# Performance work log

Hardware: AMD Instinct MI355X
Metric: run time of the kernel (lower is better)

The kernel has to match this reference:

```python
import jax, jax.numpy as jnp
import numpy as np
import math

NUM_HEADS = 16


def _alibi_slopes(num_heads: int):
    # geometric sequence for power-of-2 head counts (paper's scheme)
    def slopes_pow2(n):
        start = 2.0 ** (-(2.0 ** (-(math.log2(n) - 3))))
        return [start * (start ** i) for i in range(n)]
    if math.log2(num_heads).is_integer():
        return slopes_pow2(num_heads)
    c = 2 ** math.floor(math.log2(num_heads))
    extra = slopes_pow2(2 * c)[0::2][: num_heads - c]
    return slopes_pow2(c) + extra


def setup_inputs() -> dict:
    key = jax.random.key(0)
    kq, kk, kv = jax.random.split(key, 3)
    B, H, S, D = 2, NUM_HEADS, 2048, 64
    q = jax.random.normal(kq, (B, H, S, D), dtype=jnp.float32)
    k = jax.random.normal(kk, (B, H, S, D), dtype=jnp.float32)
    v = jax.random.normal(kv, (B, H, S, D), dtype=jnp.float32)
    return {"q": q, "k": k, "v": v}


def reference(q, k, v):
    B, H, Sq, D = q.shape
    Sk = k.shape[2]
    slopes = jnp.asarray(_alibi_slopes(H), dtype=jnp.float32)  # [H]
    pos = jnp.arange(Sk)
    # abs relative positions (symmetric, non-causal) as in the source
    rel = jnp.abs(pos[None, :] - pos[:, None]).astype(jnp.float32)  # [Sk, Sk]
    alibi = -slopes[:, None, None] * rel[None, :Sq, :]  # [H, Sq, Sk]
    scores = jnp.einsum("bhqd,bhkd->bhqk", q, k) / math.sqrt(D)
    scores = scores + alibi[None]
    probs = jax.nn.softmax(scores, axis=-1)
    return jnp.einsum("bhqk,bhkd->bhqd", probs, v)
```

## Files before the change

kernel.cpp:

```cpp
#include <hip/hip_runtime.h>
#include <hip/hip_bf16.h>
#include <math.h>

typedef __bf16 bf16;
typedef __attribute__((ext_vector_type(8))) bf16 bf16x8;
typedef __attribute__((ext_vector_type(2))) bf16 bf16x2;
typedef __attribute__((ext_vector_type(16))) float f32x16;
typedef __attribute__((ext_vector_type(4))) unsigned int uint4v;

#define SQ 2048
#define DH 64
#define NH 16
#define KVT 32
#define NKVT (SQ / KVT)
#define REC 8192
#define LOG2E 1.44269504088896340736f
#define NITEMS 1024
#define GRID 640
#define THETA 14.0f

__device__ __forceinline__ float fast_exp2(float x) {
#if __has_builtin(__builtin_amdgcn_exp2f)
    return __builtin_amdgcn_exp2f(x);
#else
    return exp2f(x);
#endif
}

__device__ __forceinline__ unsigned pkbf16(float a, float b) {
    union { bf16x2 h; unsigned u; } x;
    x.h = (bf16x2){(bf16)a, (bf16)b};
    return x.u;
}

#if __has_builtin(__builtin_amdgcn_permlane32_swap)
__device__ __forceinline__ void plswap(unsigned &a, unsigned &b) {
    typedef __attribute__((ext_vector_type(2))) unsigned int uint2v;
    uint2v r = __builtin_amdgcn_permlane32_swap(a, b, false, false);
    a = r[0]; b = r[1];
}
#else
__device__ __forceinline__ void plswap(unsigned &a, unsigned &b) {
    asm volatile("v_permlane32_swap_b32 %0, %1" : "+v"(a), "+v"(b));
}
#endif

union FragU { uint4v u; bf16x8 b; };

__global__ __launch_bounds__(256)
void alibi_prep_kernel(const float* __restrict__ K, const float* __restrict__ V,
                       char* __restrict__ W, int* __restrict__ ctr) {
    __shared__ bf16 lt[64][80];
    const int t  = threadIdx.x;
    const int s0 = blockIdx.x * 64;
    const int bh = blockIdx.y;
    if (ctr && blockIdx.x == 0 && blockIdx.y == 0 && blockIdx.z == 0 && t == 0)
        *ctr = 0;
    if (blockIdx.z == 0) {
#pragma unroll
        for (int i = 0; i < 2; ++i) {
            const int g    = i * 256 + t;
            const int tile = g >> 8;
            const int cc   = g & 255;
            const int ds   = cc >> 6;
            const int lane = cc & 63;
            const float* p = K + ((size_t)bh * SQ + s0 + tile * 32 + (lane & 31)) * DH
                               + ds * 16 + (lane >> 5) * 8;
            float4 a = *(const float4*)p, b = *(const float4*)(p + 4);
            bf16x8 pk = {(bf16)a.x,(bf16)a.y,(bf16)a.z,(bf16)a.w,
                         (bf16)b.x,(bf16)b.y,(bf16)b.z,(bf16)b.w};
            *(bf16x8*)(W + (size_t)(bh * NKVT + (s0 >> 5) + tile) * REC
                         + ds * 1024 + lane * 16) = pk;
        }
    } else {
#pragma unroll
        for (int i = 0; i < 2; ++i) {
            int idx = i * 256 + t;
            int row = idx >> 3, c8 = idx & 7;
            const float* p = V + ((size_t)bh * SQ + s0 + row) * DH + c8 * 8;
            float4 a = *(const float4*)p, b = *(const float4*)(p + 4);
            bf16 e[8] = {(bf16)a.x,(bf16)a.y,(bf16)a.z,(bf16)a.w,
                         (bf16)b.x,(bf16)b.y,(bf16)b.z,(bf16)b.w};
#pragma unroll
            for (int jj = 0; jj < 8; ++jj) lt[c8 * 8 + jj][row] = e[jj];
        }
        __syncthreads();
#pragma unroll
        for (int i = 0; i < 2; ++i) {
            const int g    = i * 256 + t;
            const int tile = g >> 8;
            const int cc   = g & 255;
            const int grp  = cc >> 6;
            const int lane = cc & 63;
            const int d    = (grp >> 1) * 32 + (lane & 31);
            const int sv   = tile * 32 + (grp & 1) * 16 + (lane >> 5) * 8;
            bf16x8 v = *(const bf16x8*)&lt[d][sv];
            *(bf16x8*)(W + (size_t)(bh * NKVT + (s0 >> 5) + tile) * REC
                         + 4096 + grp * 1024 + lane * 16) = v;
        }
    }
}

__global__ __launch_bounds__(256, 2)
void alibi_attn_kernel(const float* __restrict__ Q, const char* __restrict__ W,
                       float* __restrict__ Out, int* __restrict__ ctr) {
    __shared__ float ex[2][64][72];
    __shared__ int s_id;
    const int tid  = threadIdx.x;
    const int lane = tid & 63;
    const int par  = tid >> 6;
    const int r32  = lane & 31;
    const int hi   = lane >> 5;
    const float QSCALE = 0.125f * LOG2E;

    int next_static = blockIdx.x;

    while (true) {
        if (tid == 0) s_id = ctr ? atomicAdd(ctr, 1) : next_static;
        __syncthreads();
        const int r = s_id;
        next_static += GRID;
        if (r >= NITEMS) break;

        const int h   = 15 - (r >> 6);
        const int sub = r & 63;
        const int bh  = (sub >> 5) * NH + h;
        const int q0  = (sub & 31) * 64;

        const float slope2  = exp2f(-0.5f * (float)(h + 1)) * LOG2E;
        const float SLOPE2N = -slope2;
        const int D = (int)(THETA / slope2);
        const int a0 = q0 - D;
        const int tmin = (a0 <= 0) ? 0 : (a0 >> 5);
        const int tmax = min(NKVT - 1, (q0 + 63 + D) >> 5);

        const float* Qp = Q + (size_t)bh * SQ * DH;
        float*       Op = Out + (size_t)bh * SQ * DH;
        const char*  rec = W + (size_t)bh * NKVT * REC;

        const int qrowA = q0 + r32;
        bf16x8 qfragA[4], qfragB[4];
#pragma unroll
        for (int ds = 0; ds < 4; ++ds) {
            const float* sa = Qp + (size_t)qrowA * DH + ds * 16 + hi * 8;
            float4 a = *(const float4*)sa, b = *(const float4*)(sa + 4);
            qfragA[ds] = (bf16x8){(bf16)(a.x*QSCALE),(bf16)(a.y*QSCALE),
                                  (bf16)(a.z*QSCALE),(bf16)(a.w*QSCALE),
                                  (bf16)(b.x*QSCALE),(bf16)(b.y*QSCALE),
                                  (bf16)(b.z*QSCALE),(bf16)(b.w*QSCALE)};
            const float* sb = sa + 32 * DH;
            float4 c = *(const float4*)sb, d = *(const float4*)(sb + 4);
            qfragB[ds] = (bf16x8){(bf16)(c.x*QSCALE),(bf16)(c.y*QSCALE),
                                  (bf16)(c.z*QSCALE),(bf16)(c.w*QSCALE),
                                  (bf16)(d.x*QSCALE),(bf16)(d.y*QSCALE),
                                  (bf16)(d.z*QSCALE),(bf16)(d.w*QSCALE)};
        }

        f32x16 oaccA[2], oaccB[2];
#pragma unroll
        for (int d2 = 0; d2 < 2; ++d2)
#pragma unroll
            for (int rr = 0; rr < 16; ++rr) { oaccA[d2][rr] = 0.f; oaccB[d2][rr] = 0.f; }
        float psA[4] = {0.f,0.f,0.f,0.f}, psB[4] = {0.f,0.f,0.f,0.f};
        const float qhA = (float)(qrowA - 4 * hi);

        auto LOADF = [&](bf16x8* kf, bf16x8* vf, int tt) {
            const char* rb = rec + (size_t)tt * REC + lane * 16;
#pragma unroll
            for (int ds = 0; ds < 4; ++ds) kf[ds] = *(const bf16x8*)(rb + ds * 1024);
#pragma unroll
            for (int g = 0; g < 4; ++g)    vf[g] = *(const bf16x8*)(rb + 4096 + g * 1024);
        };

        auto COMPUTE = [&](const bf16x8* kf, const bf16x8* vf, int tt) {
            const float gq0 = qhA - (float)(tt * KVT);
#pragma unroll
            for (int qs = 0; qs < 2; ++qs) {
                const bf16x8* qf = qs ? qfragB : qfragA;
                f32x16*       oa = qs ? oaccB  : oaccA;
                float*        ps = qs ? psB    : psA;
                const float   gq = qs ? gq0 + 32.f : gq0;

                f32x16 sacc;
#pragma unroll
                for (int rr = 0; rr < 16; ++rr) sacc[rr] = 0.f;
                __builtin_amdgcn_s_setprio(1);
#pragma unroll
                for (int ds = 0; ds < 4; ++ds)
                    sacc = __builtin_amdgcn_mfma_f32_32x32x16_bf16(kf[ds], qf[ds], sacc, 0, 0, 0);
                __builtin_amdgcn_s_setprio(0);

                float p[16];
#pragma unroll
                for (int reg = 0; reg < 16; ++reg) {
                    const int krel = (reg & 3) + 8 * (reg >> 2);
                    float d = gq - (float)krel;
                    float s2 = fmaf(SLOPE2N, fabsf(d), sacc[reg]);
                    float e = fast_exp2(s2);
                    p[reg] = e;
                    ps[reg & 3] += e;
                }

                __builtin_amdgcn_s_setprio(1);
#pragma unroll
                for (int ks = 0; ks < 2; ++ks) {
                    unsigned u0 = pkbf16(p[8 * ks + 0], p[8 * ks + 1]);
                    unsigned u1 = pkbf16(p[8 * ks + 2], p[8 * ks + 3]);
                    unsigned v0 = pkbf16(p[8 * ks + 4], p[8 * ks + 5]);
                    unsigned v1 = pkbf16(p[8 * ks + 6], p[8 * ks + 7]);
                    plswap(u0, v0);
                    plswap(u1, v1);
                    FragU pf; pf.u = (uint4v){u0, u1, v0, v1};
#pragma unroll
                    for (int dblk = 0; dblk < 2; ++dblk)
                        oa[dblk] = __builtin_amdgcn_mfma_f32_32x32x16_bf16(vf[dblk * 2 + ks], pf.b, oa[dblk], 0, 0, 0);
                }
                __builtin_amdgcn_s_setprio(0);
            }
        };

        {
            bf16x8 kA[4], vA[4], kB[4], vB[4];
            int t = tmin + par;
            if (t <= tmax) {
                const int n = ((tmax - t) >> 2) + 1;
                LOADF(kA, vA, t);
                int i = 0;
                while (i + 2 <= n) {
                    LOADF(kB, vB, t + 4);
                    asm volatile("s_waitcnt vmcnt(8)" ::: "memory");
                    __builtin_amdgcn_sched_barrier(0);
                    COMPUTE(kA, vA, t);
                    if (i + 2 < n) {
                        LOADF(kA, vA, t + 8);
                        asm volatile("s_waitcnt vmcnt(8)" ::: "memory");
                    } else {
                        asm volatile("s_waitcnt vmcnt(0)" ::: "memory");
                    }
                    __builtin_amdgcn_sched_barrier(0);
                    COMPUTE(kB, vB, t + 4);
                    t += 8; i += 2;
                }
                if (i < n) {
                    asm volatile("s_waitcnt vmcnt(0)" ::: "memory");
                    __builtin_amdgcn_sched_barrier(0);
                    COMPUTE(kA, vA, t);
                }
            }
        }

        float psumA = (psA[0] + psA[1]) + (psA[2] + psA[3]);
        psumA += __shfl_xor(psumA, 32);
        float psumB = (psB[0] + psB[1]) + (psB[2] + psB[3]);
        psumB += __shfl_xor(psumB, 32);

        auto WRITE = [&](int si) {
            float* s = &ex[si][lane][0];
#pragma unroll
            for (int dblk = 0; dblk < 2; ++dblk)
#pragma unroll
                for (int g2 = 0; g2 < 4; ++g2) {
                    *(float4*)(s + dblk * 16 + g2 * 4) =
                        (float4){oaccA[dblk][4*g2+0], oaccA[dblk][4*g2+1],
                                 oaccA[dblk][4*g2+2], oaccA[dblk][4*g2+3]};
                    *(float4*)(s + 36 + dblk * 16 + g2 * 4) =
                        (float4){oaccB[dblk][4*g2+0], oaccB[dblk][4*g2+1],
                                 oaccB[dblk][4*g2+2], oaccB[dblk][4*g2+3]};
                }
            s[32] = psumA;
            s[68] = psumB;
        };
        auto ADDIN = [&](int si) {
            const float* s = &ex[si][lane][0];
#pragma unroll
            for (int dblk = 0; dblk < 2; ++dblk)
#pragma unroll
                for (int g2 = 0; g2 < 4; ++g2) {
                    float4 oa = *(const float4*)(s + dblk * 16 + g2 * 4);
                    float4 ob = *(const float4*)(s + 36 + dblk * 16 + g2 * 4);
                    oaccA[dblk][4*g2+0] += oa.x; oaccA[dblk][4*g2+1] += oa.y;
                    oaccA[dblk][4*g2+2] += oa.z; oaccA[dblk][4*g2+3] += oa.w;
                    oaccB[dblk][4*g2+0] += ob.x; oaccB[dblk][4*g2+1] += ob.y;
                    oaccB[dblk][4*g2+2] += ob.z; oaccB[dblk][4*g2+3] += ob.w;
                }
            psumA += s[32];
            psumB += s[68];
        };

        if (par & 1) WRITE(par >> 1);
        __syncthreads();
        if (!(par & 1)) ADDIN(par >> 1);
        __syncthreads();
        if (par == 2) WRITE(0);
        __syncthreads();
        if (par == 0) {
            ADDIN(0);
            const float invA = 1.f / psumA;
            const float invB = 1.f / psumB;
#pragma unroll
            for (int dblk = 0; dblk < 2; ++dblk)
#pragma unroll
                for (int g2 = 0; g2 < 4; ++g2) {
                    float4 oa = {oaccA[dblk][4*g2+0] * invA, oaccA[dblk][4*g2+1] * invA,
                                 oaccA[dblk][4*g2+2] * invA, oaccA[dblk][4*g2+3] * invA};
                    *(float4*)(Op + (size_t)qrowA * DH + dblk * 32 + g2 * 8 + hi * 4) = oa;
                    float4 ob = {oaccB[dblk][4*g2+0] * invB, oaccB[dblk][4*g2+1] * invB,
                                 oaccB[dblk][4*g2+2] * invB, oaccB[dblk][4*g2+3] * invB};
                    *(float4*)(Op + (size_t)(qrowA + 32) * DH + dblk * 32 + g2 * 8 + hi * 4) = ob;
                }
        }
    }
}

extern "C" void kernel_launch(void* const* d_in, const int* in_sizes, int n_in,
                              void* d_out, int out_size, void* d_ws, size_t ws_size,
                              hipStream_t stream) {
    const float* q = (const float*)d_in[0];
    const float* k = (const float*)d_in[1];
    const float* v = (const float*)d_in[2];
    float* out = (float*)d_out;
    char* W = (char*)d_ws;
    const size_t rec_bytes = (size_t)32 * NKVT * REC;
    int* ctr = (ws_size >= rec_bytes + 4) ? (int*)((char*)d_ws + rec_bytes) : nullptr;
    alibi_prep_kernel<<<dim3(SQ / 64, 2 * NH, 2), dim3(256), 0, stream>>>(k, v, W, ctr);
    alibi_attn_kernel<<<dim3(GRID), dim3(256), 0, stream>>>(q, W, out, ctr);
}
```

Before: 49.78 us.

## Split KV range for high-window heads and add a partial-sum reduce kernel

Work items for the five heads with the widest ALiBi window are split into two halves of the KV tile range. Each half writes unnormalized partial outputs and row sums to a workspace buffer, and a new reduce kernel adds the two halves and normalizes. The other heads keep the original single-pass path, and the grid grows to 1024 blocks. The aim is to balance the long items so the tail of the persistent loop shrinks. In exchange it adds an extra kernel launch, partial-result global traffic and more workspace use. It relies on both halves sharing a max-free exp2 formulation so their sums can simply be added.

After: 63.26 us. 27.1% more time.

```diff
diff --git a/kernel.cpp b/kernel.cpp
--- a/kernel.cpp
+++ b/kernel.cpp
@@ -15,9 +15,11 @@
 #define NKVT (SQ / KVT)
 #define REC 8192
 #define LOG2E 1.44269504088896340736f
-#define NITEMS 1024
-#define GRID 640
 #define THETA 14.0f
+#define SPLIT_RANKS 640
+#define NIT_SPLIT 1344
+#define NIT_FLAT 1024
+#define SLOTF 4160
 
 __device__ __forceinline__ float fast_exp2(float x) {
 #if __has_builtin(__builtin_amdgcn_exp2f)
@@ -101,9 +103,35 @@
     }
 }
 
+__global__ __launch_bounds__(256)
+void alibi_reduce_kernel(const float* __restrict__ P, float* __restrict__ Out) {
+    const int i  = blockIdx.x;
+    const int hh = i >> 6;
+    const int h  = 15 - hh;
+    const int sub = i & 63;
+    const int bh = (sub >> 5) * NH + h;
+    const int q0 = (sub & 31) * 64;
+    const float* s0 = P + (size_t)(2 * i) * SLOTF;
+    const float* s1 = s0 + SLOTF;
+    float* Op = Out + ((size_t)bh * SQ + q0) * DH;
+    const int t  = threadIdx.x;
+    const int q  = t >> 2;
+    const int d0 = (t & 3) * 16;
+    const float inv = 1.f / (s0[4096 + q] + s1[4096 + q]);
+#pragma unroll
+    for (int d = 0; d < 16; d += 4) {
+        float4 a = *(const float4*)(s0 + q * 64 + d0 + d);
+        float4 b = *(const float4*)(s1 + q * 64 + d0 + d);
+        float4 o = {(a.x + b.x) * inv, (a.y + b.y) * inv,
+                    (a.z + b.z) * inv, (a.w + b.w) * inv};
+        *(float4*)(Op + (size_t)q * DH + d0 + d) = o;
+    }
+}
+
 __global__ __launch_bounds__(256, 2)
 void alibi_attn_kernel(const float* __restrict__ Q, const char* __restrict__ W,
-                       float* __restrict__ Out, int* __restrict__ ctr) {
+                       float* __restrict__ Out, int* __restrict__ ctr,
+                       float* __restrict__ Pbuf, int split) {
     __shared__ float ex[2][64][72];
     __shared__ int s_id;
     const int tid  = threadIdx.x;
@@ -112,6 +140,7 @@
     const int r32  = lane & 31;
     const int hi   = lane >> 5;
     const float QSCALE = 0.125f * LOG2E;
+    const int NIT = split ? NIT_SPLIT : NIT_FLAT;
 
     int next_static = blockIdx.x;
 
@@ -119,23 +148,34 @@
         if (tid == 0) s_id = ctr ? atomicAdd(ctr, 1) : next_static;
         __syncthreads();
         const int r = s_id;
-        next_static += GRID;
-        if (r >= NITEMS) break;
-
-        const int h   = 15 - (r >> 6);
-        const int sub = r & 63;
-        const int bh  = (sub >> 5) * NH + h;
-        const int q0  = (sub & 31) * 64;
+        next_static += gridDim.x;
+        if (r >= NIT) break;
+
+        int h, sub, seg, nseg;
+        if (split && r < SPLIT_RANKS) {
+            h = 15 - (r >> 7); sub = (r >> 1) & 63; seg = r & 1; nseg = 2;
+        } else if (split) {
+            const int rl = r - SPLIT_RANKS;
+            h = 10 - (rl >> 6); sub = rl & 63; seg = 0; nseg = 1;
+        } else {
+            h = 15 - (r >> 6); sub = r & 63; seg = 0; nseg = 1;
+        }
+        const int bh = (sub >> 5) * NH + h;
+        const int q0 = (sub & 31) * 64;
 
         const float slope2  = exp2f(-0.5f * (float)(h + 1)) * LOG2E;
         const float SLOPE2N = -slope2;
         const int D = (int)(THETA / slope2);
         const int a0 = q0 - D;
-        const int tmin = (a0 <= 0) ? 0 : (a0 >> 5);
-        const int tmax = min(NKVT - 1, (q0 + 63 + D) >> 5);
+        int tmin = (a0 <= 0) ? 0 : (a0 >> 5);
+        int tmax = min(NKVT - 1, (q0 + 63 + D) >> 5);
+        if (nseg == 2) {
+            const int T = tmax - tmin + 1;
+            const int tmid = tmin + ((T + 1) >> 1);
+            if (seg == 0) tmax = tmid - 1; else tmin = tmid;
+        }
 
         const float* Qp = Q + (size_t)bh * SQ * DH;
-        float*       Op = Out + (size_t)bh * SQ * DH;
         const char*  rec = W + (size_t)bh * NKVT * REC;
 
         const int qrowA = q0 + r32;
@@ -295,19 +335,39 @@
         __syncthreads();
         if (par == 0) {
             ADDIN(0);
-            const float invA = 1.f / psumA;
-            const float invB = 1.f / psumB;
-#pragma unroll
-            for (int dblk = 0; dblk < 2; ++dblk)
-#pragma unroll
-                for (int g2 = 0; g2 < 4; ++g2) {
-                    float4 oa = {oaccA[dblk][4*g2+0] * invA, oaccA[dblk][4*g2+1] * invA,
-                                 oaccA[dblk][4*g2+2] * invA, oaccA[dblk][4*g2+3] * invA};
-                    *(float4*)(Op + (size_t)qrowA * DH + dblk * 32 + g2 * 8 + hi * 4) = oa;
-                    float4 ob = {oaccB[dblk][4*g2+0] * invB, oaccB[dblk][4*g2+1] * invB,
-                                 oaccB[dblk][4*g2+2] * invB, oaccB[dblk][4*g2+3] * invB};
-                    *(float4*)(Op + (size_t)(qrowA + 32) * DH + dblk * 32 + g2 * 8 + hi * 4) = ob;
-                }
+            if (nseg == 2) {
+                float* slot = Pbuf + (size_t)r * SLOTF;
+#pragma unroll
+                for (int dblk = 0; dblk < 2; ++dblk)
+#pragma unroll
+                    for (int g2 = 0; g2 < 4; ++g2) {
+                        *(float4*)(slot + r32 * 64 + dblk * 32 + g2 * 8 + hi * 4) =
+                            (float4){oaccA[dblk][4*g2+0], oaccA[dblk][4*g2+1],
+                                     oaccA[dblk][4*g2+2], oaccA[dblk][4*g2+3]};
+                        *(float4*)(slot + (r32 + 32) * 64 + dblk * 32 + g2 * 8 + hi * 4) =
+                            (float4){oaccB[dblk][4*g2+0], oaccB[dblk][4*g2+1],
+                                     oaccB[dblk][4*g2+2], oaccB[dblk][4*g2+3]};
+                    }
+                if (hi == 0) {
+                    slot[4096 + r32] = psumA;
+                    slot[4128 + r32] = psumB;
+                }
+            } else {
+                float* Op = Out + (size_t)bh * SQ * DH;
+                const float invA = 1.f / psumA;
+                const float invB = 1.f / psumB;
+#pragma unroll
+                for (int dblk = 0; dblk < 2; ++dblk)
+#pragma unroll
+                    for (int g2 = 0; g2 < 4; ++g2) {
+                        float4 oa = {oaccA[dblk][4*g2+0] * invA, oaccA[dblk][4*g2+1] * invA,
+                                     oaccA[dblk][4*g2+2] * invA, oaccA[dblk][4*g2+3] * invA};
+                        *(float4*)(Op + (size_t)qrowA * DH + dblk * 32 + g2 * 8 + hi * 4) = oa;
+                        float4 ob = {oaccB[dblk][4*g2+0] * invB, oaccB[dblk][4*g2+1] * invB,
+                                     oaccB[dblk][4*g2+2] * invB, oaccB[dblk][4*g2+3] * invB};
+                        *(float4*)(Op + (size_t)(qrowA + 32) * DH + dblk * 32 + g2 * 8 + hi * 4) = ob;
+                    }
+            }
         }
     }
 }
@@ -320,8 +380,16 @@
     const float* v = (const float*)d_in[2];
     float* out = (float*)d_out;
     char* W = (char*)d_ws;
-    const size_t rec_bytes = (size_t)32 * NKVT * REC;
-    int* ctr = (ws_size >= rec_bytes + 4) ? (int*)((char*)d_ws + rec_bytes) : nullptr;
+    const size_t rec_bytes  = (size_t)32 * NKVT * REC;
+    const size_t part_bytes = (size_t)SPLIT_RANKS * SLOTF * sizeof(float);
+    const int split = (ws_size >= rec_bytes + part_bytes + 64) ? 1 : 0;
+    float* Pbuf = (float*)(W + rec_bytes);
+    int*   ctr  = (int*)(W + rec_bytes + (split ? part_bytes : 0));
+    if (ws_size < rec_bytes + 4) ctr = nullptr;
+
     alibi_prep_kernel<<<dim3(SQ / 64, 2 * NH, 2), dim3(256), 0, stream>>>(k, v, W, ctr);
-    alibi_attn_kernel<<<dim3(GRID), dim3(256), 0, stream>>>(q, W, out, ctr);
-}
+    const int grid = split ? 1024 : 640;
+    alibi_attn_kernel<<<dim3(grid), dim3(256), 0, stream>>>(q, W, out, ctr, Pbuf, split);
+    if (split)
+        alibi_reduce_kernel<<<dim3(SPLIT_RANKS / 2), dim3(256), 0, stream>>>(Pbuf, out);
+}
```
